# Kernel tuning notes

Hardware: AMD Instinct MI355X
Metric: run time of the kernel (lower is better)

The kernel has to match this reference:

```python
import jax, jax.numpy as jnp
import numpy as np
from jax.scipy.special import logsumexp

B, N1, N2, D = 32, 512, 512, 128
M_WARP = 256   # n_warp_fn_times
M_DISCR = 96   # n_warp_discr (warp-value grid per time step)
GAMMA = 0.1    # softmin temperature (soft relaxation of the hard-argmin GDTW DP)
BARRIER = 1e4  # soft penalty enforcing endpoint + local-gradient constraints


def setup_inputs() -> dict:
    key = jax.random.key(0)
    k1, k2, k3 = jax.random.split(key, 3)
    return {
        "signal1_features": jax.random.normal(k1, (B, N1, D), jnp.float32),
        "signal2_features": jax.random.normal(k2, (B, N2, D), jnp.float32),
        "reg_wt": jax.random.uniform(k3, (B,), jnp.float32, 0.1, 1.0),
        "glb_lb": jnp.zeros((B, M_WARP), jnp.float32),
        "glb_ub": jnp.ones((B, M_WARP), jnp.float32),
        "lcl_grad_ub": 2.0 * jnp.ones((B, 1), jnp.float32),
        "signal1_times": jnp.broadcast_to(jnp.linspace(0.0, 1.0, N1, dtype=jnp.float32)[None], (B, N1)),
        "signal2_times": jnp.broadcast_to(jnp.linspace(0.0, 1.0, N2, dtype=jnp.float32)[None], (B, N2)),
        "warp_fn_times": jnp.broadcast_to(jnp.linspace(0.0, 1.0, M_WARP, dtype=jnp.float32)[None], (B, M_WARP)),
    }


def _interp_uniform(feats, pos):
    """Linear interpolation of feats [b,n,d] at normalized positions pos in [0,1]."""
    b, n, d = feats.shape
    shp = pos.shape
    x = jnp.clip(pos, 0.0, 1.0) * (n - 1)
    i0 = jnp.clip(x.astype(jnp.int32), 0, n - 2)
    w = (x - i0.astype(x.dtype)).reshape(b, -1, 1)
    flat = i0.reshape(b, -1)
    f0 = jnp.take_along_axis(feats, flat[..., None], axis=1)
    f1 = jnp.take_along_axis(feats, flat[..., None] + 1, axis=1)
    return (f0 * (1.0 - w) + f1 * w).reshape(*shp, d)


def _softmin(x, axis):
    return -GAMMA * logsumexp(-x / GAMMA, axis=axis)


def _gdtw(s1f, s2f, reg_wt, glb_lb, glb_ub, lcl_grad_ub, t1, t2, tw):
    b, m = tw.shape
    T2 = jnp.max(t2, axis=1, keepdims=True)                       # [b,1]
    lb = glb_lb * T2
    ub = glb_ub * T2
    frac = jnp.linspace(0.0, 1.0, M_DISCR, dtype=tw.dtype)
    tau = lb[..., None] + (ub - lb)[..., None] * frac             # [b,m,M] candidate warp values
    s1_at = _interp_uniform(s1f, tw / jnp.max(t1, axis=1, keepdims=True))  # [b,m,d]
    s2_at = _interp_uniform(s2f, tau / T2[..., None])             # [b,m,M,d]
    diff = s1_at[:, :, None, :] - s2_at
    dtw_ = jnp.diff(tw, axis=1)                                   # [b,m-1]
    wts = 0.5 * jnp.concatenate([dtw_[:, :1], dtw_[:, 1:] + dtw_[:, :-1], dtw_[:, -1:]], axis=1)
    node = jnp.sum(diff * diff, axis=-1) * wts[..., None]         # [b,m,M] feature loss (p=2), trapezoid dt
    # endpoint constraints (subseq_enabled=False): phi(t0)=0, phi(tm)=T2
    node = node.at[:, 0].add(BARRIER * tau[:, 0] ** 2)
    node = node.at[:, -1].add(BARRIER * (tau[:, -1] - T2) ** 2)
    # transition costs: regularisation |phi' - 1|^2 dt + soft barriers for 0 <= phi' <= lcl_grad_ub
    slope = (tau[:, 1:, None, :] - tau[:, :-1, :, None]) / dtw_[:, :, None, None]  # [b,m-1,Mk,Mj]
    gub = lcl_grad_ub[:, :, None, None]
    pen = BARRIER * (jax.nn.relu(-slope) ** 2 + jax.nn.relu(slope - gub) ** 2)
    edge = reg_wt[:, None, None, None] * (slope - 1.0) ** 2 * dtw_[:, :, None, None] + pen
    edge_sc = jnp.moveaxis(edge, 1, 0)                            # [m-1,b,M,M]
    node_sc = jnp.moveaxis(node[:, 1:], 1, 0)                     # [m-1,b,M]

    def fwd_step(a, x):
        n_i, e_i = x
        a_new = n_i + _softmin(a[:, :, None] + e_i, axis=1)
        return a_new, a_new

    a0 = node[:, 0]
    _, alphas = jax.lax.scan(fwd_step, a0, (node_sc, edge_sc))
    alpha = jnp.concatenate([a0[None], alphas], axis=0)           # [m,b,M]

    def bwd_step(bn, x):
        n_ip1, e_i = x
        b_new = _softmin(e_i + (n_ip1 + bn)[:, None, :], axis=2)
        return b_new, b_new

    bT = jnp.zeros_like(a0)
    _, betas = jax.lax.scan(bwd_step, bT, (node_sc, edge_sc), reverse=True)
    beta = jnp.concatenate([betas, bT[None]], axis=0)             # [m,b,M]

    p = jax.nn.softmax(-(alpha + beta) / GAMMA, axis=-1)          # node marginals [m,b,M]
    return jnp.einsum('mbk,bmk->bm', p, tau)                      # expected warp values [b,m]


def reference(signal1_features, signal2_features, reg_wt, glb_lb, glb_ub, lcl_grad_ub, signal1_times, signal2_times, warp_fn_times):
    return _gdtw(signal1_features, signal2_features, reg_wt, glb_lb, glb_ub, lcl_grad_ub,
                 signal1_times, signal2_times, warp_fn_times)
```

## Files before the change

### kernel.cpp

```cpp
#include <hip/hip_runtime.h>

#define NB 32
#define N1 512
#define N2 512
#define DF 128
#define MW 256
#define KD 96
#define INVG 10.0f
#define GAM 0.1f
#define BARRIER 10000.0f

#define WS_NODE  0
#define WS_ABUF  (WS_NODE + NB*MW*KD)
#define WS_BBUF  (WS_ABUF + NB*MW*KD)

__device__ __forceinline__ bool feq(float a, float b) {
  return fabsf(a - b) <= 1e-4f * fmaxf(fabsf(a), fabsf(b)) + 1e-12f;
}

__device__ __forceinline__ float edgec(float s, float rdtv, float gub) {
  float d = s - 1.0f, ng = fminf(s, 0.f), ov = fmaxf(s - gub, 0.f);
  return rdtv*d*d + BARRIER*(ng*ng + ov*ov);
}

__device__ __forceinline__ float dpp_shr1(float x) {
  return __int_as_float(__builtin_amdgcn_update_dpp(
      0, __float_as_int(x), 0x138, 0xf, 0xf, true));
}
__device__ __forceinline__ float dpp_shl1(float x) {
  return __int_as_float(__builtin_amdgcn_update_dpp(
      0, __float_as_int(x), 0x130, 0xf, 0xf, true));
}

__global__ __launch_bounds__(256) void k1_node(const float* __restrict__ s1f,
                                               const float* __restrict__ s2f,
                                               const float* __restrict__ tw,
                                               const float* __restrict__ glb_lb,
                                               const float* __restrict__ glb_ub,
                                               const float* __restrict__ t1,
                                               const float* __restrict__ t2,
                                               float* __restrict__ ws) {
  const int mb = blockIdx.x;
  const int b  = blockIdx.y;
  const int t  = threadIdx.x;
  const int lane = t & 63;
  const int wv = t >> 6;
  __shared__ float s1L[16*132];
  __shared__ float s2L[96*132];
  __shared__ float ndt[16*99];
  __shared__ float wtsL[16], lbL[16], ubL[16];
  __shared__ int   matchL[16];
  __shared__ float redm[8];

  {
    float m1 = -1e30f, m2 = -1e30f;
    for (int i = t; i < N1; i += 256) m1 = fmaxf(m1, t1[b*N1+i]);
    for (int i = t; i < N2; i += 256) m2 = fmaxf(m2, t2[b*N2+i]);
    #pragma unroll
    for (int o = 32; o; o >>= 1) {
      m1 = fmaxf(m1, __shfl_down(m1, o));
      m2 = fmaxf(m2, __shfl_down(m2, o));
    }
    if (lane == 0) { redm[wv] = m1; redm[4+wv] = m2; }
  }
  __syncthreads();
  const float T1 = fmaxf(fmaxf(redm[0], redm[1]), fmaxf(redm[2], redm[3]));
  const float T2 = fmaxf(fmaxf(redm[4], redm[5]), fmaxf(redm[6], redm[7]));
  const float lb0 = glb_lb[b*MW] * T2;
  const float ub0 = glb_ub[b*MW] * T2;
  float4* s1L4 = (float4*)s1L;
  float4* s2L4 = (float4*)s2L;
  const float4* s1f4 = (const float4*)(s1f + (size_t)b*N1*DF);
  const float4* s2f4 = (const float4*)(s2f + (size_t)b*N2*DF);

  {
    const int d32 = t & 31;
    const int k8  = t >> 5;
    #pragma unroll
    for (int kk = 0; kk < 12; kk++) {
      int k = k8 + 8*kk;
      float tau = lb0 + (ub0 - lb0) * (float)k * (1.0f/95.0f);
      float x = fminf(fmaxf(tau / T2, 0.f), 1.f) * (float)(N2-1);
      int i0 = (int)x; i0 = max(0, min(i0, N2-2));
      float w = x - (float)i0;
      float4 f0 = s2f4[(size_t)i0*32 + d32];
      float4 f1 = s2f4[(size_t)(i0+1)*32 + d32];
      float4 r;
      r.x = f0.x + (f1.x - f0.x)*w; r.y = f0.y + (f1.y - f0.y)*w;
      r.z = f0.z + (f1.z - f0.z)*w; r.w = f0.w + (f1.w - f0.w)*w;
      s2L4[k*33 + d32] = r;
    }
  }
  {
    const int smi = t >> 4, q = t & 15;
    const int m = mb*16 + smi;
    float twm = tw[b*MW + m];
    float x = fminf(fmaxf(twm / T1, 0.f), 1.f) * (float)(N1-1);
    int i0 = (int)x; i0 = max(0, min(i0, N1-2));
    float w = x - (float)i0;
    #pragma unroll
    for (int j = 0; j < 2; j++) {
      int d4 = q + 16*j;
      float4 f0 = s1f4[(size_t)i0*32 + d4];
      float4 f1 = s1f4[(size_t)(i0+1)*32 + d4];
      float4 r;
      r.x = f0.x + (f1.x - f0.x)*w; r.y = f0.y + (f1.y - f0.y)*w;
      r.z = f0.z + (f1.z - f0.z)*w; r.w = f0.w + (f1.w - f0.w)*w;
      s1L4[smi*33 + d4] = r;
    }
  }
  if (t < 16) {
    int m = mb*16 + t, g = b*MW + m;
    float twm = tw[g];
    float prev = (m > 0) ? tw[g-1] : twm;
    float next = (m < MW-1) ? tw[g+1] : twm;
    wtsL[t] = 0.5f*(next - prev);
    float lbm = glb_lb[g]*T2, ubm = glb_ub[g]*T2;
    lbL[t] = lbm; ubL[t] = ubm;
    matchL[t] = (feq(lbm, lb0) && feq(ubm, ub0)) ? 1 : 0;
  }
  __syncthreads();

  const int mi = t >> 4, kg = t & 15;
  const int m = mb*16 + mi;
  float acc[6];
  #pragma unroll
  for (int i = 0; i < 6; i++) acc[i] = 0.f;
  if (matchL[mi]) {
    for (int d4 = 0; d4 < 32; d4++) {
      float4 s1v = s1L4[mi*33 + d4];
      #pragma unroll
      for (int k12 = 0; k12 < 6; k12++) {
        int k = kg + 16*k12;
        float4 s2v = s2L4[k*33 + d4];
        float dx = s1v.x - s2v.x, dy = s1v.y - s2v.y;
        float dz = s1v.z - s2v.z, dw = s1v.w - s2v.w;
        acc[k12] += dx*dx + dy*dy + dz*dz + dw*dw;
      }
    }
  } else {
    const float lbm = lbL[mi], ubm = ubL[mi];
    int i0a[6]; float wa[6];
    #pragma unroll
    for (int k12 = 0; k12 < 6; k12++) {
      int k = kg + 16*k12;
      float tau = lbm + (ubm - lbm) * (float)k * (1.0f/95.0f);
      float x = fminf(fmaxf(tau / T2, 0.f), 1.f) * (float)(N2-1);
      int i0 = (int)x; i0 = max(0, min(i0, N2-2));
      i0a[k12] = i0; wa[k12] = x - (float)i0;
    }
    for (int d4 = 0; d4 < 32; d4++) {
      float4 s1v = s1L4[mi*33 + d4];
      #pragma unroll
      for (int k12 = 0; k12 < 6; k12++) {
        float4 f0 = s2f4[(size_t)i0a[k12]*32 + d4];
        float4 f1 = s2f4[(size_t)(i0a[k12]+1)*32 + d4];
        float w = wa[k12];
        float ax = f0.x + (f1.x - f0.x)*w, ay = f0.y + (f1.y - f0.y)*w;
        float az = f0.z + (f1.z - f0.z)*w, aw = f0.w + (f1.w - f0.w)*w;
        float dx = s1v.x - ax, dy = s1v.y - ay, dz = s1v.z - az, dw = s1v.w - aw;
        acc[k12] += dx*dx + dy*dy + dz*dz + dw*dw;
      }
    }
  }
  {
    const float wts = wtsL[mi];
    const float lbm = lbL[mi], ubm = ubL[mi];
    #pragma unroll
    for (int k12 = 0; k12 < 6; k12++) {
      int k = kg + 16*k12;
      float nodev = acc[k12] * wts;
      float tau = lbm + (ubm - lbm) * (float)k * (1.0f/95.0f);
      if (m == 0)    nodev += BARRIER * tau * tau;
      if (m == MW-1) { float dd = tau - T2; nodev += BARRIER * dd * dd; }
      ndt[mi*99 + k] = nodev;
    }
  }
  __syncthreads();
  float* nodeP = ws + WS_NODE + ((size_t)b*MW + mb*16)*KD;
  for (int idx = t; idx < 16*KD; idx += 256) {
    int mi2 = idx / KD, kv = idx - mi2*KD;
    nodeP[idx] = ndt[mi2*99 + kv];
  }
}

__global__ __launch_bounds__(512) void k2_out(const float* __restrict__ tw,
                                              const float* __restrict__ glb_lb,
                                              const float* __restrict__ glb_ub,
                                              const float* __restrict__ reg_wt,
                                              const float* __restrict__ gubp,
                                              const float* __restrict__ t2,
                                              float* __restrict__ ws,
                                              float* __restrict__ out) {
  const int b = blockIdx.x;
  const int t = threadIdx.x;
  const int wv = t >> 6;
  const int lane = t & 63;
  __shared__ float ndL[MW*KD];
  __shared__ float ndmL[MW];
  __shared__ float lbw[MW], ubw[MW], twv[MW];
  __shared__ float mir[2][KD];
  __shared__ float sred[32];
  __shared__ int skey[8];
  const float* __restrict__ nodeP = ws + WS_NODE + (size_t)b*MW*KD;

  {
    const float4* np4 = (const float4*)nodeP;
    float4* nl4 = (float4*)ndL;
    #pragma unroll
    for (int it = 0; it < (MW*KD/4)/512; it++)
      nl4[t + 512*it] = np4[t + 512*it];
  }
  {
    float m2 = -1e30f;
    for (int i = t; i < N2; i += 512) m2 = fmaxf(m2, t2[b*N2+i]);
    #pragma unroll
    for (int o = 32; o; o >>= 1) m2 = fmaxf(m2, __shfl_down(m2, o));
    if (lane == 0) sred[wv] = m2;
  }
  __syncthreads();
  float T2;
  {
    float v = sred[0];
    #pragma unroll
    for (int w = 1; w < 8; w++) v = fmaxf(v, sred[w]);
    T2 = v;
  }
  for (int i = t; i < MW; i += 512) {
    lbw[i] = glb_lb[b*MW+i]*T2;
    ubw[i] = glb_ub[b*MW+i]*T2;
    twv[i] = tw[b*MW+i];
  }
  const float r = reg_wt[b];
  const float gub = gubp[b];
  __syncthreads();

  const float lb0 = lbw[0], ub0 = ubw[0];
  const float g = (ub0 - lb0) * (1.0f/95.0f);
  bool keyok = true;
  float minE1 = 3e38f, minE2 = 3e38f, maxRdt = 0.f;
  for (int i = t; i < MW; i += 512)
    keyok = keyok && (lbw[i] == lb0) && (ubw[i] == ub0);
  for (int i = t; i < MW-1; i += 512) {
    float dtv = twv[i+1] - twv[i];
    if (!(dtv > 0.f)) keyok = false;
    else {
      float rdtv = r * dtv, sl = g / dtv;
      minE1 = fminf(minE1, fminf(edgec(sl, rdtv, gub), edgec(-sl, rdtv, gub)));
      minE2 = fminf(minE2, fminf(edgec(2.f*sl, rdtv, gub), edgec(-2.f*sl, rdtv, gub)));
      maxRdt = fmaxf(maxRdt, rdtv);
    }
  }

  const bool actS = t < KD;
  const int k = actS ? t : (KD-1);
  float P = 0.f, mx = 0.f;
  if (t < 128) {
    const bool hasn = actS && (k < KD-1);
    float P2 = 0.f;
    #pragma unroll 8
    for (int m = 0; m < MW; m++) {
      float a  = ndL[m*KD + k];
      float bq = hasn ? ndL[m*KD + k + 1] : a;
      P += a; P2 += bq;
      mx = fmaxf(mx, fabsf(P - P2));
    }
    if (!actS) mx = 0.f;
  }
  {
    float wmx = mx, wE1 = minE1, wE2 = minE2, wR = maxRdt;
    #pragma unroll
    for (int o = 32; o; o >>= 1) {
      wmx = fmaxf(wmx, __shfl_xor(wmx, o));
      wE1 = fminf(wE1, __shfl_xor(wE1, o));
      wE2 = fminf(wE2, __shfl_xor(wE2, o));
      wR  = fmaxf(wR,  __shfl_xor(wR,  o));
    }
    int ka = __all(keyok ? 1 : 0);
    if (lane == 0) {
      sred[wv*4+0] = wmx; sred[wv*4+1] = wE1;
      sred[wv*4+2] = wE2; sred[wv*4+3] = wR;
      skey[wv] = ka;
    }
  }
  __syncthreads();
  float MX, E1, E2, RD; int KAll;
  {
    float a0 = sred[0], a1 = sred[1], a2 = sred[2], a3 = sred[3];
    int kk2 = skey[0];
    #pragma unroll
    for (int w = 1; w < 8; w++) {
      a0 = fmaxf(a0, sred[w*4+0]);
      a1 = fminf(a1, sred[w*4+1]);
      a2 = fminf(a2, sred[w*4+2]);
      a3 = fmaxf(a3, sred[w*4+3]);
      kk2 = kk2 && skey[w];
    }
    MX = a0; E1 = a1; E2 = a2; RD = a3; KAll = kk2;
  }
  const bool ok = KAll &&
                  (2.0f*MX   <= E1 - RD - 3.0f) &&
                  (190.0f*MX <= E2 - RD - 3.0f);

  if (ok) {
    __syncthreads();
    float s = actS ? P : 3e38f;
    float mnv = s;
    #pragma unroll
    for (int o = 32; o; o >>= 1) mnv = fminf(mnv, __shfl_xor(mnv, o));
    if (lane == 0) sred[wv] = mnv;
    __syncthreads();
    float mn;
    {
      float v = sred[0];
      #pragma unroll
      for (int w = 1; w < 8; w++) v = fminf(v, sred[w]);
      mn = v;
    }
    float w = actS ? __expf((mn - P) * INVG) : 0.f;
    float num = w * (float)k, den = w;
    #pragma unroll
    for (int o = 32; o; o >>= 1) {
      num += __shfl_xor(num, o);
      den += __shfl_xor(den, o);
    }
    if (lane == 0) { sred[8+wv] = num; sred[16+wv] = den; }
    __syncthreads();
    float nsum, dsum;
    {
      float n0 = sred[8], d0 = sred[16];
      #pragma unroll
      for (int w2 = 1; w2 < 8; w2++) { n0 += sred[8+w2]; d0 += sred[16+w2]; }
      nsum = n0; dsum = d0;
    }
    const float q = (nsum / dsum) * (1.0f/95.0f);
    for (int m = t; m < MW; m += 512)
      out[b*MW + m] = lbw[m] + (ubw[m] - lbw[m]) * q;
    return;
  }

  {
    for (int i2 = t; i2 < MW; i2 += 512) {
      float mnv = 3e38f;
      for (int kk = 0; kk < KD; kk++) mnv = fminf(mnv, ndL[i2*KD + kk]);
      ndmL[i2] = mnv;
    }
    __syncthreads();

    if (t < 128) {
      const int dir = t >> 6;
      const bool act = lane < 48;
      const int k0i = 2*lane, k1i = 2*lane+1;
      const float frk0 = (float)k0i*(1.f/95.f), frk1 = (float)k1i*(1.f/95.f);
      float* __restrict__ outP = ws + (dir ? WS_BBUF : WS_ABUF) + (size_t)b*MW*KD;

      float a0 = 3e38f, a1 = 3e38f;
      {
        const int m0 = dir ? (MW-1) : 0;
        if (act) {
          a0 = ndL[m0*KD + k0i]; a1 = ndL[m0*KD + k1i];
          mir[dir][k0i] = a0; mir[dir][k1i] = a1;
          float2 o; o.x = dir ? 0.f : a0; o.y = dir ? 0.f : a1;
          *(float2*)&outP[(size_t)m0*KD + k0i] = o;
        }
      }
      float Blo;
      {
        float bl = act ? fminf(a0, a1) : 3e38f;
        #pragma unroll
        for (int o = 1; o < 64; o <<= 1) bl = fminf(bl, __shfl_xor(bl, o));
        Blo = bl;
      }
      float e00=3e38f,e0m=3e38f,e0p=3e38f,e10=3e38f,e1m=3e38f,e1p=3e38f;
      float eo0=3e38f, eo1=3e38f, eminmin=0.f;
      float cL1=__int_as_float(0x7fc00000), cU1=cL1, cL2=cL1, cU2=cL1, cdt=cL1;

      float pL1, pU1, pL2, pU2, pt1, pt2, pnd0=0.f, pnd1=0.f, pndm;
      {
        const int i0_ = dir ? (MW-2) : 0;
        pL1=lbw[i0_]; pU1=ubw[i0_]; pL2=lbw[i0_+1]; pU2=ubw[i0_+1];
        pt1=twv[i0_]; pt2=twv[i0_+1];
        const int mn_ = dir ? i0_ : (i0_+1);
        if (act) { float2 v = *(const float2*)&ndL[mn_*KD + k0i]; pnd0=v.x; pnd1=v.y; }
        pndm = ndmL[mn_];
      }

      for (int step = 0; step < MW-1; step++) {
        const float L1=pL1, U1=pU1, L2=pL2, U2=pU2;
        const float dt = pt2 - pt1;
        const float nd0=pnd0, nd1=pnd1, ndmn=pndm;
        {
          const int sn = (step+1 < MW-1) ? (step+1) : step;
          const int in_ = dir ? (MW-2-sn) : sn;
          pL1=lbw[in_]; pU1=ubw[in_]; pL2=lbw[in_+1]; pU2=ubw[in_+1];
          pt1=twv[in_]; pt2=twv[in_+1];
          const int mn_ = dir ? in_ : (in_+1);
          if (act) { float2 v = *(const float2*)&ndL[mn_*KD + k0i]; pnd0=v.x; pnd1=v.y; }
          pndm = ndmL[mn_];
        }
        const bool kc = !(feq(L1,cL1)&&feq(U1,cU1)&&feq(L2,cL2)&&feq(U2,cU2)&&feq(dt,cdt));
        if (kc) {
          cL1=L1; cU1=U1; cL2=L2; cU2=U2; cdt=dt;
          float bl = act ? fminf(mir[dir][k0i], mir[dir][k1i]) : 3e38f;
          #pragma unroll
          for (int o = 1; o < 64; o <<= 1) bl = fminf(bl, __shfl_xor(bl, o));
          Blo = bl;
          const float invdt = 1.f/dt, rdt = r*dt;
          const float my0 = dir ? (L1+(U1-L1)*frk0) : (L2+(U2-L2)*frk0);
          const float my1 = dir ? (L1+(U1-L1)*frk1) : (L2+(U2-L2)*frk1);
          e00=3e38f; e0m=3e38f; e0p=3e38f; e10=3e38f; e1m=3e38f; e1p=3e38f;
          eo0=3e38f; eo1=3e38f;
          float emn = 3e38f;
          for (int j = 0; j < KD; j++) {
            const float frj = (float)j*(1.f/95.f);
            const float oth = dir ? (L2+(U2-L2)*frj) : (L1+(U1-L1)*frj);
            const float sl0 = (dir ? (oth-my0) : (my0-oth))*invdt;
            const float sl1 = (dir ? (oth-my1) : (my1-oth))*invdt;
            float d0=sl0-1.f, g0=fminf(sl0,0.f), v0=fmaxf(sl0-gub,0.f);
            float ej0 = rdt*d0*d0 + BARRIER*(g0*g0+v0*v0);
            float d1=sl1-1.f, g1=fminf(sl1,0.f), v1=fmaxf(sl1-gub,0.f);
            float ej1 = rdt*d1*d1 + BARRIER*(g1*g1+v1*v1);
            emn = fminf(emn, fminf(ej0, ej1));
            if      (j == k0i-1) e0m = ej0;
            else if (j == k0i)   e00 = ej0;
            else if (j == k0i+1) e0p = ej0;
            else                 eo0 = fminf(eo0, ej0);
            if      (j == k1i-1) e1m = ej1;
            else if (j == k1i)   e10 = ej1;
            else if (j == k1i+1) e1p = ej1;
            else                 eo1 = fminf(eo1, ej1);
          }
          if (!act) emn = 3e38f;
          #pragma unroll
          for (int o = 1; o < 64; o <<= 1) emn = fminf(emn, __shfl_xor(emn, o));
          eminmin = emn;
        }
        const float a1p = dpp_shr1(a1);
        const float a0n = dpp_shl1(a0);
        const float x0m = fminf(a1p + e0m, 3e38f);
        const float x00 = fminf(a0  + e00, 3e38f);
        const float x0p = fminf(a1  + e0p, 3e38f);
        const float x1m = fminf(a0  + e1m, 3e38f);
        const float x10 = fminf(a1  + e10, 3e38f);
        const float x1p = fminf(a0n + e1p, 3e38f);
        float mn0 = fminf(fminf(x0m, x00), x0p);
        float mn1 = fminf(fminf(x1m, x10), x1p);
        float sum0 = __expf((mn0-x0m)*INVG) + __expf((mn0-x00)*INVG) + __expf((mn0-x0p)*INVG);
        float sum1 = __expf((mn1-x1m)*INVG) + __expf((mn1-x10)*INVG) + __expf((mn1-x1p)*INVG);
        const bool bad = act && ((Blo + eo0 - mn0 < 8.7f) || (Blo + eo1 - mn1 < 8.7f));
        if (__any((int)bad)) {
          const float invdt = 1.f/dt, rdt = r*dt;
          const float my0 = dir ? (L1+(U1-L1)*frk0) : (L2+(U2-L2)*frk0);
          const float my1 = dir ? (L1+(U1-L1)*frk1) : (L2+(U2-L2)*frk1);
          mn0 = 3e38f; mn1 = 3e38f;
          for (int j = 0; j < KD; j++) {
            const float sj = mir[dir][j];
            const float frj = (float)j*(1.f/95.f);
            const float oth = dir ? (L2+(U2-L2)*frj) : (L1+(U1-L1)*frj);
            const float sl0 = (dir ? (oth-my0) : (my0-oth))*invdt;
            const float sl1 = (dir ? (oth-my1) : (my1-oth))*invdt;
            float d0=sl0-1.f, g0=fminf(sl0,0.f), v0=fmaxf(sl0-gub,0.f);
            float ej0 = rdt*d0*d0 + BARRIER*(g0*g0+v0*v0);
            float d1=sl1-1.f, g1=fminf(sl1,0.f), v1=fmaxf(sl1-gub,0.f);
            float ej1 = rdt*d1*d1 + BARRIER*(g1*g1+v1*v1);
            mn0 = fminf(mn0, fminf(sj + ej0, 3e38f));
            mn1 = fminf(mn1, fminf(sj + ej1, 3e38f));
          }
          sum0 = 0.f; sum1 = 0.f;
          for (int j = 0; j < KD; j++) {
            const float sj = mir[dir][j];
            const float frj = (float)j*(1.f/95.f);
            const float oth = dir ? (L2+(U2-L2)*frj) : (L1+(U1-L1)*frj);
            const float sl0 = (dir ? (oth-my0) : (my0-oth))*invdt;
            const float sl1 = (dir ? (oth-my1) : (my1-oth))*invdt;
            float d0=sl0-1.f, g0=fminf(sl0,0.f), v0=fmaxf(sl0-gub,0.f);
            float ej0 = rdt*d0*d0 + BARRIER*(g0*g0+v0*v0);
            float d1=sl1-1.f, g1=fminf(sl1,0.f), v1=fmaxf(sl1-gub,0.f);
            float ej1 = rdt*d1*d1 + BARRIER*(g1*g1+v1*v1);
            sum0 += __expf((mn0 - fminf(sj + ej0, 3e38f))*INVG);
            sum1 += __expf((mn1 - fminf(sj + ej1, 3e38f))*INVG);
          }
        }
        const float sv0 = mn0 - GAM*__logf(sum0);
        const float sv1 = mn1 - GAM*__logf(sum1);
        const float na0 = nd0 + sv0, na1 = nd1 + sv1;
        const int ic = dir ? (MW-2-step) : step;
        const int mnode = dir ? ic : (ic+1);
        if (act) {
          mir[dir][k0i] = na0; mir[dir][k1i] = na1;
          float2 o; o.x = dir ? sv0 : na0; o.y = dir ? sv1 : na1;
          *(float2*)&outP[(size_t)mnode*KD + k0i] = o;
        }
        a0 = act ? na0 : 3e38f;
        a1 = act ? na1 : 3e38f;
        Blo += eminmin + ndmn - 0.4575f;
      }
    }

    __threadfence_block();
    __syncthreads();
    const float* __restrict__ Ab = ws + WS_ABUF + (size_t)b*MW*KD;
    const float* __restrict__ Bb = ws + WS_BBUF + (size_t)b*MW*KD;
    for (int m = t; m < MW; m += 512) {
      float mnv = 3e38f;
      for (int kk = 0; kk < KD; kk++)
        mnv = fminf(mnv, Ab[(size_t)m*KD+kk] + Bb[(size_t)m*KD+kk]);
      float num = 0.f, den = 0.f;
      for (int kk = 0; kk < KD; kk++) {
        float s = Ab[(size_t)m*KD+kk] + Bb[(size_t)m*KD+kk];
        float w = __expf((mnv - s) * INVG);
        num += w * (float)kk; den += w;
      }
      out[b*MW + m] = lbw[m] + (ubw[m] - lbw[m]) * (num/den) * (1.0f/95.0f);
    }
  }
}

extern "C" void kernel_launch(void* const* d_in, const int* in_sizes, int n_in,
                              void* d_out, int out_size, void* d_ws, size_t ws_size,
                              hipStream_t stream) {
  const float* s1f    = (const float*)d_in[0];
  const float* s2f    = (const float*)d_in[1];
  const float* regw   = (const float*)d_in[2];
  const float* glb_lb = (const float*)d_in[3];
  const float* glb_ub = (const float*)d_in[4];
  const float* gubp   = (const float*)d_in[5];
  const float* t1     = (const float*)d_in[6];
  const float* t2     = (const float*)d_in[7];
  const float* twp    = (const float*)d_in[8];
  float* ws  = (float*)d_ws;
  float* out = (float*)d_out;

  dim3 g1(16, NB);
  k1_node<<<g1, 256, 0, stream>>>(s1f, s2f, twp, glb_lb, glb_ub, t1, t2, ws);
  k2_out<<<NB, 512, 0, stream>>>(twp, glb_lb, glb_ub, regw, gubp, t2, ws, out);
}
```

Before: 108.0 us.

## Register-tile node cost over two rows, pack DP params, vectorize marginal loops

The node-cost kernel now has each thread compute two warp-time rows against three candidates, so every s2 LDS load is reused twice. The DP loop reads a precomputed packed float4 of bounds plus dt instead of six scalar LDS loads per step. Redundant clamps on the candidate sums are removed. The row-min pass is rotated per lane to avoid LDS bank conflicts, and the final marginal loops read float4. These are several small latency reductions, and dropping the clamps could yield inf/NaN if costs overflow.

```diff
diff --git a/kernel.cpp b/kernel.cpp
--- a/kernel.cpp
+++ b/kernel.cpp
@@ -121,59 +121,87 @@
   }
   __syncthreads();
 
-  const int mi = t >> 4, kg = t & 15;
-  const int m = mb*16 + mi;
-  float acc[6];
+  const int mp = t >> 5, kt = t & 31;
+  const int mi0 = 2*mp, mi1 = mi0 + 1;
+  float acc0[3], acc1[3];
   #pragma unroll
-  for (int i = 0; i < 6; i++) acc[i] = 0.f;
-  if (matchL[mi]) {
+  for (int i = 0; i < 3; i++) { acc0[i] = 0.f; acc1[i] = 0.f; }
+
+  if (matchL[mi0] && matchL[mi1]) {
     for (int d4 = 0; d4 < 32; d4++) {
-      float4 s1v = s1L4[mi*33 + d4];
+      float4 s1a = s1L4[mi0*33 + d4];
+      float4 s1b = s1L4[mi1*33 + d4];
       #pragma unroll
-      for (int k12 = 0; k12 < 6; k12++) {
-        int k = kg + 16*k12;
-        float4 s2v = s2L4[k*33 + d4];
-        float dx = s1v.x - s2v.x, dy = s1v.y - s2v.y;
-        float dz = s1v.z - s2v.z, dw = s1v.w - s2v.w;
-        acc[k12] += dx*dx + dy*dy + dz*dz + dw*dw;
+      for (int j = 0; j < 3; j++) {
+        float4 s2v = s2L4[(kt + 32*j)*33 + d4];
+        float dx = s1a.x - s2v.x, dy = s1a.y - s2v.y;
+        float dz = s1a.z - s2v.z, dw = s1a.w - s2v.w;
+        acc0[j] += dx*dx + dy*dy + dz*dz + dw*dw;
+        float ex = s1b.x - s2v.x, ey = s1b.y - s2v.y;
+        float ez = s1b.z - s2v.z, ew = s1b.w - s2v.w;
+        acc1[j] += ex*ex + ey*ey + ez*ez + ew*ew;
       }
     }
   } else {
-    const float lbm = lbL[mi], ubm = ubL[mi];
-    int i0a[6]; float wa[6];
-    #pragma unroll
-    for (int k12 = 0; k12 < 6; k12++) {
-      int k = kg + 16*k12;
-      float tau = lbm + (ubm - lbm) * (float)k * (1.0f/95.0f);
-      float x = fminf(fmaxf(tau / T2, 0.f), 1.f) * (float)(N2-1);
-      int i0 = (int)x; i0 = max(0, min(i0, N2-2));
-      i0a[k12] = i0; wa[k12] = x - (float)i0;
-    }
-    for (int d4 = 0; d4 < 32; d4++) {
-      float4 s1v = s1L4[mi*33 + d4];
+    #pragma unroll 1
+    for (int rr = 0; rr < 2; rr++) {
+      const int mi = mi0 + rr;
+      float* accp = rr ? acc1 : acc0;
+      if (matchL[mi]) {
+        for (int d4 = 0; d4 < 32; d4++) {
+          float4 s1v = s1L4[mi*33 + d4];
+          #pragma unroll
+          for (int j = 0; j < 3; j++) {
+            float4 s2v = s2L4[(kt + 32*j)*33 + d4];
+            float dx = s1v.x - s2v.x, dy = s1v.y - s2v.y;
+            float dz = s1v.z - s2v.z, dw = s1v.w - s2v.w;
+            accp[j] += dx*dx + dy*dy + dz*dz + dw*dw;
+          }
+        }
+      } else {
+        const float lbm = lbL[mi], ubm = ubL[mi];
+        int i0a[3]; float wa[3];
+        #pragma unroll
+        for (int j = 0; j < 3; j++) {
+          int k = kt + 32*j;
+          float tau = lbm + (ubm - lbm) * (float)k * (1.0f/95.0f);
+          float x = fminf(fmaxf(tau / T2, 0.f), 1.f) * (float)(N2-1);
+          int i0 = (int)x; i0 = max(0, min(i0, N2-2));
+          i0a[j] = i0; wa[j] = x - (float)i0;
+        }
+        for (int d4 = 0; d4 < 32; d4++) {
+          float4 s1v = s1L4[mi*33 + d4];
+          #pragma unroll
+          for (int j = 0; j < 3; j++) {
+            float4 f0 = s2f4[(size_t)i0a[j]*32 + d4];
+            float4 f1 = s2f4[(size_t)(i0a[j]+1)*32 + d4];
+            float w = wa[j];
+            float ax = f0.x + (f1.x - f0.x)*w, ay = f0.y + (f1.y - f0.y)*w;
+            float az = f0.z + (f1.z - f0.z)*w, aw = f0.w + (f1.w - f0.w)*w;
+            float dx = s1v.x - ax, dy = s1v.y - ay, dz = s1v.z - az, dw = s1v.w - aw;
+            accp[j] += dx*dx + dy*dy + dz*dz + dw*dw;
+          }
+        }
+      }
+    }
+  }
+  {
+    #pragma unroll
+    for (int rr = 0; rr < 2; rr++) {
+      const int mi = mi0 + rr;
+      const int m = mb*16 + mi;
+      const float wts = wtsL[mi];
+      const float lbm = lbL[mi], ubm = ubL[mi];
+      float* accp = rr ? acc1 : acc0;
       #pragma unroll
-      for (int k12 = 0; k12 < 6; k12++) {
-        float4 f0 = s2f4[(size_t)i0a[k12]*32 + d4];
-        float4 f1 = s2f4[(size_t)(i0a[k12]+1)*32 + d4];
-        float w = wa[k12];
-        float ax = f0.x + (f1.x - f0.x)*w, ay = f0.y + (f1.y - f0.y)*w;
-        float az = f0.z + (f1.z - f0.z)*w, aw = f0.w + (f1.w - f0.w)*w;
-        float dx = s1v.x - ax, dy = s1v.y - ay, dz = s1v.z - az, dw = s1v.w - aw;
-        acc[k12] += dx*dx + dy*dy + dz*dz + dw*dw;
-      }
-    }
-  }
-  {
-    const float wts = wtsL[mi];
-    const float lbm = lbL[mi], ubm = ubL[mi];
-    #pragma unroll
-    for (int k12 = 0; k12 < 6; k12++) {
-      int k = kg + 16*k12;
-      float nodev = acc[k12] * wts;
-      float tau = lbm + (ubm - lbm) * (float)k * (1.0f/95.0f);
-      if (m == 0)    nodev += BARRIER * tau * tau;
-      if (m == MW-1) { float dd = tau - T2; nodev += BARRIER * dd * dd; }
-      ndt[mi*99 + k] = nodev;
+      for (int j = 0; j < 3; j++) {
+        int k = kt + 32*j;
+        float nodev = accp[j] * wts;
+        float tau = lbm + (ubm - lbm) * (float)k * (1.0f/95.0f);
+        if (m == 0)    nodev += BARRIER * tau * tau;
+        if (m == MW-1) { float dd = tau - T2; nodev += BARRIER * dd * dd; }
+        ndt[mi*99 + k] = nodev;
+      }
     }
   }
   __syncthreads();
@@ -199,6 +227,8 @@
   __shared__ float ndL[MW*KD];
   __shared__ float ndmL[MW];
   __shared__ float lbw[MW], ubw[MW], twv[MW];
+  __shared__ float4 prmL[MW];
+  __shared__ float dtL[MW];
   __shared__ float mir[2][KD];
   __shared__ float sred[32];
   __shared__ int skey[8];
@@ -340,10 +370,21 @@
   }
 
   {
-    for (int i2 = t; i2 < MW; i2 += 512) {
+    for (int i = t; i < MW-1; i += 512) {
+      float4 p; p.x = lbw[i]; p.y = ubw[i]; p.z = lbw[i+1]; p.w = ubw[i+1];
+      prmL[i] = p;
+      dtL[i] = twv[i+1] - twv[i];
+    }
+    if (t < MW) {
+      const float* rowp = &ndL[t*KD];
       float mnv = 3e38f;
-      for (int kk = 0; kk < KD; kk++) mnv = fminf(mnv, ndL[i2*KD + kk]);
-      ndmL[i2] = mnv;
+      int c = lane;
+      #pragma unroll 8
+      for (int j = 0; j < KD; j++) {
+        mnv = fminf(mnv, rowp[c]);
+        c++; if (c >= KD) c -= KD;
+      }
+      ndmL[t] = mnv;
     }
     __syncthreads();
 
@@ -375,25 +416,23 @@
       float eo0=3e38f, eo1=3e38f, eminmin=0.f;
       float cL1=__int_as_float(0x7fc00000), cU1=cL1, cL2=cL1, cU2=cL1, cdt=cL1;
 
-      float pL1, pU1, pL2, pU2, pt1, pt2, pnd0=0.f, pnd1=0.f, pndm;
+      float4 pprm; float pdt; float pnd0=0.f, pnd1=0.f, pndm;
       {
         const int i0_ = dir ? (MW-2) : 0;
-        pL1=lbw[i0_]; pU1=ubw[i0_]; pL2=lbw[i0_+1]; pU2=ubw[i0_+1];
-        pt1=twv[i0_]; pt2=twv[i0_+1];
+        pprm = prmL[i0_]; pdt = dtL[i0_];
         const int mn_ = dir ? i0_ : (i0_+1);
         if (act) { float2 v = *(const float2*)&ndL[mn_*KD + k0i]; pnd0=v.x; pnd1=v.y; }
         pndm = ndmL[mn_];
       }
 
       for (int step = 0; step < MW-1; step++) {
-        const float L1=pL1, U1=pU1, L2=pL2, U2=pU2;
-        const float dt = pt2 - pt1;
+        const float L1=pprm.x, U1=pprm.y, L2=pprm.z, U2=pprm.w;
+        const float dt = pdt;
         const float nd0=pnd0, nd1=pnd1, ndmn=pndm;
         {
           const int sn = (step+1 < MW-1) ? (step+1) : step;
           const int in_ = dir ? (MW-2-sn) : sn;
-          pL1=lbw[in_]; pU1=ubw[in_]; pL2=lbw[in_+1]; pU2=ubw[in_+1];
-          pt1=twv[in_]; pt2=twv[in_+1];
+          pprm = prmL[in_]; pdt = dtL[in_];
           const int mn_ = dir ? in_ : (in_+1);
           if (act) { float2 v = *(const float2*)&ndL[mn_*KD + k0i]; pnd0=v.x; pnd1=v.y; }
           pndm = ndmL[mn_];
@@ -437,12 +476,12 @@
         }
         const float a1p = dpp_shr1(a1);
         const float a0n = dpp_shl1(a0);
-        const float x0m = fminf(a1p + e0m, 3e38f);
-        const float x00 = fminf(a0  + e00, 3e38f);
-        const float x0p = fminf(a1  + e0p, 3e38f);
-        const float x1m = fminf(a0  + e1m, 3e38f);
-        const float x10 = fminf(a1  + e10, 3e38f);
-        const float x1p = fminf(a0n + e1p, 3e38f);
+        const float x0m = a1p + e0m;
+        const float x00 = a0  + e00;
+        const float x0p = a1  + e0p;
+        const float x1m = a0  + e1m;
+        const float x10 = a1  + e10;
+        const float x1p = a0n + e1p;
         float mn0 = fminf(fminf(x0m, x00), x0p);
         float mn1 = fminf(fminf(x1m, x10), x1p);
         float sum0 = __expf((mn0-x0m)*INVG) + __expf((mn0-x00)*INVG) + __expf((mn0-x0p)*INVG);
@@ -502,14 +541,27 @@
     const float* __restrict__ Ab = ws + WS_ABUF + (size_t)b*MW*KD;
     const float* __restrict__ Bb = ws + WS_BBUF + (size_t)b*MW*KD;
     for (int m = t; m < MW; m += 512) {
+      const float4* Ab4 = (const float4*)&Ab[(size_t)m*KD];
+      const float4* Bb4 = (const float4*)&Bb[(size_t)m*KD];
       float mnv = 3e38f;
-      for (int kk = 0; kk < KD; kk++)
-        mnv = fminf(mnv, Ab[(size_t)m*KD+kk] + Bb[(size_t)m*KD+kk]);
+      #pragma unroll 4
+      for (int q = 0; q < KD/4; q++) {
+        float4 av = Ab4[q], bv = Bb4[q];
+        mnv = fminf(mnv, fminf(fminf(av.x+bv.x, av.y+bv.y),
+                               fminf(av.z+bv.z, av.w+bv.w)));
+      }
       float num = 0.f, den = 0.f;
-      for (int kk = 0; kk < KD; kk++) {
-        float s = Ab[(size_t)m*KD+kk] + Bb[(size_t)m*KD+kk];
-        float w = __expf((mnv - s) * INVG);
-        num += w * (float)kk; den += w;
+      #pragma unroll 4
+      for (int q = 0; q < KD/4; q++) {
+        float4 av = Ab4[q], bv = Bb4[q];
+        float w0 = __expf((mnv - (av.x+bv.x)) * INVG);
+        float w1 = __expf((mnv - (av.y+bv.y)) * INVG);
+        float w2 = __expf((mnv - (av.z+bv.z)) * INVG);
+        float w3 = __expf((mnv - (av.w+bv.w)) * INVG);
+        num += w0 * (float)(4*q+0); den += w0;
+        num += w1 * (float)(4*q+1); den += w1;
+        num += w2 * (float)(4*q+2); den += w2;
+        num += w3 * (float)(4*q+3); den += w3;
       }
       out[b*MW + m] = lbw[m] + (ubw[m] - lbw[m]) * (num/den) * (1.0f/95.0f);
     }
```

After: 106.5 us. Within noise of the previous version (-1.4%).
